# Kernel tuning notes

Measured on AMD Instinct MI355X. Metric: run time of the kernel, lower is better.

Reference implementation:

```python
import jax, jax.numpy as jnp
import numpy as np

BATCH, L, IN_DIM, HID, STATE, MLP, OUT, NUM_LAYERS = 16, 2048, 64, 256, 256, 1024, 128, 4
MAX_PHASE = 2.0 * np.pi


def setup_inputs() -> dict:
    key = jax.random.key(0)
    ks = iter(jax.random.split(key, 32))
    x = jax.random.normal(next(ks), (BATCH, L, IN_DIM), dtype=jnp.float32)
    # embedding Linear(IN_DIM -> HID)
    emb_W = jax.random.normal(next(ks), (HID, IN_DIM), dtype=jnp.float32) / np.sqrt(IN_DIM)
    emb_b = jnp.zeros((HID,), dtype=jnp.float32)
    # LRU params per layer (r_min=0, r_max=1, max_phase=2pi)
    u1 = jax.random.uniform(next(ks), (NUM_LAYERS, STATE), minval=1e-4, maxval=1.0)
    u2 = jax.random.uniform(next(ks), (NUM_LAYERS, STATE), minval=1e-4, maxval=1.0)
    nu_log = jnp.log(-0.5 * jnp.log(u1))
    theta_log = jnp.log(MAX_PHASE * u2)
    lam_abs = jnp.exp(-jnp.exp(nu_log))
    gamma_log = jnp.log(jnp.sqrt(1.0 - lam_abs ** 2))
    B_re = jax.random.normal(next(ks), (NUM_LAYERS, STATE, HID)) / np.sqrt(2 * HID)
    B_im = jax.random.normal(next(ks), (NUM_LAYERS, STATE, HID)) / np.sqrt(2 * HID)
    C_re = jax.random.normal(next(ks), (NUM_LAYERS, HID, STATE)) / np.sqrt(STATE)
    C_im = jax.random.normal(next(ks), (NUM_LAYERS, HID, STATE)) / np.sqrt(STATE)
    D = jax.random.normal(next(ks), (NUM_LAYERS, HID))
    # block MLP: Linear(STATE->MLP), GELU, Linear(MLP->HID)
    Wh = jax.random.normal(next(ks), (NUM_LAYERS, MLP, STATE)) / np.sqrt(STATE)
    bh = jnp.zeros((NUM_LAYERS, MLP), dtype=jnp.float32)
    Wo = jax.random.normal(next(ks), (NUM_LAYERS, HID, MLP)) / np.sqrt(MLP)
    bo = jnp.zeros((NUM_LAYERS, HID), dtype=jnp.float32)
    # output Linear(HID -> OUT)
    out_W = jax.random.normal(next(ks), (OUT, HID), dtype=jnp.float32) / np.sqrt(HID)
    out_b = jnp.zeros((OUT,), dtype=jnp.float32)
    return {"x": x, "emb_W": emb_W, "emb_b": emb_b, "nu_log": nu_log,
            "theta_log": theta_log, "gamma_log": gamma_log, "B_re": B_re,
            "B_im": B_im, "C_re": C_re, "C_im": C_im, "D": D,
            "Wh": Wh, "bh": bh, "Wo": Wo, "bo": bo,
            "out_W": out_W, "out_b": out_b}


def _binop(ei, ej):
    a_i, bu_i = ei
    a_j, bu_j = ej
    return a_j * a_i, a_j * bu_i + bu_j


def _lru(x, nu, th, gl, Bre, Bim, Cre, Cim, D):
    # x: (B, L, H) real; state diag recurrence in complex64
    lam = jnp.exp(-jnp.exp(nu) + 1j * jnp.exp(th))               # (S,)
    B_norm = (Bre + 1j * Bim) * jnp.exp(gl)[:, None]             # (S, H)
    Bu = jnp.einsum("blh,sh->bls", x.astype(B_norm.dtype), B_norm)  # (B, L, S)
    Lam = jnp.broadcast_to(lam, Bu.shape)
    _, states = jax.lax.associative_scan(_binop, (Lam, Bu), axis=1)
    C = Cre + 1j * Cim                                           # (H, S)
    y = jnp.einsum("bls,hs->blh", states, C).real + D * x        # (B, L, H)
    return y


def reference(x, emb_W, emb_b, nu_log, theta_log, gamma_log, B_re, B_im,
              C_re, C_im, D, Wh, bh, Wo, bo, out_W, out_b):
    h = x @ emb_W.T + emb_b                                      # (B, L, HID)
    for l in range(NUM_LAYERS):
        y = _lru(h, nu_log[l], theta_log[l], gamma_log[l],
                 B_re[l], B_im[l], C_re[l], C_im[l], D[l])
        z = jax.nn.gelu(y @ Wh[l].T + bh[l], approximate=False)  # exact GELU as torch
        h = z @ Wo[l].T + bo[l] + y                              # residual
    return h @ out_W.T + out_b                                   # (B, L, OUT)
```

## Files before the change

### kernel.cpp

```cpp
#include <hip/hip_runtime.h>
#include <hip/hip_bf16.h>
#include <math.h>

typedef __hip_bfloat16 bf16;
typedef __attribute__((ext_vector_type(8))) short bf16x8;
typedef __attribute__((ext_vector_type(4))) float f32x4;

#define BATCH   16
#define SEQLEN  2048
#define INDIM   64
#define HIDD    256
#define STATE_D 256
#define MLPD    1024
#define OUTD    128
#define NLAYERS 4
#define M_TOK   (BATCH*SEQLEN)
#define CHUNK   64
#define NCHUNK  (SEQLEN/CHUNK)

__device__ float g_carry[512*512];
__device__ bf16  g_hb [(size_t)M_TOK*256];
__device__ bf16  g_yb [(size_t)M_TOK*256];
__device__ bf16  g_bub[(size_t)M_TOK*512];
__device__ bf16  g_Bnb[NLAYERS*512*256];
__device__ bf16  g_Cwb[NLAYERS*256*512];
__device__ bf16  g_Whb[NLAYERS*1024*256];
__device__ bf16  g_Wob[NLAYERS*256*1024];

#define SB_HB  0
#define SB_YB  1
#define SB_BUB 2
#define SB_BNB 4
#define SB_CWB 5
#define SB_WHB 6
#define SB_WOB 7

__device__ __forceinline__ bf16* bufb(int sel){
  switch(sel){
    case SB_HB:  return g_hb;  case SB_YB:  return g_yb;
    case SB_BUB: return g_bub;
    case SB_BNB: return g_Bnb; case SB_CWB: return g_Cwb;
    case SB_WHB: return g_Whb; default:     return g_Wob; }
}

__device__ __forceinline__ void gld_lds16(const void* g, void* l){
  __builtin_amdgcn_global_load_lds(
      (const __attribute__((address_space(1))) unsigned int*)g,
      (__attribute__((address_space(3))) unsigned int*)l, 16, 0, 0);
}

__device__ __forceinline__ float fast_gelu(float v){
  const float x  = v * 0.70710678118654752f;
  const float ax = fabsf(x);
  const float t  = __builtin_amdgcn_rcpf(fmaf(0.3275911f, ax, 1.0f));
  float p = fmaf(t, 1.061405429f, -1.453152027f);
  p = fmaf(t, p, 1.421413741f);
  p = fmaf(t, p, -0.284496736f);
  p = fmaf(t, p, 0.254829592f);
  p = p * t;
  const float e = __expf(-ax * ax);
  const float erf_ax = fmaf(-p, e, 1.0f);
  const float erf_x  = copysignf(erf_ax, x);
  return 0.5f * v * (1.0f + erf_x);
}

__device__ __forceinline__ unsigned int bf2_add(unsigned int a, unsigned int b){
  float alo = __uint_as_float(a << 16), ahi = __uint_as_float(a & 0xffff0000u);
  float blo = __uint_as_float(b << 16), bhi = __uint_as_float(b & 0xffff0000u);
  bf16 l = __float2bfloat16(alo + blo);
  bf16 h = __float2bfloat16(ahi + bhi);
  return (unsigned int)(*reinterpret_cast<unsigned short*>(&l))
       | ((unsigned int)(*reinterpret_cast<unsigned short*>(&h)) << 16);
}

__device__ __forceinline__ void lam_of(const float* __restrict__ nu_log,
                                       const float* __restrict__ th_log,
                                       int s, float& lr, float& li)
{
  float nu  = expf(nu_log[s]);
  float th  = expf(th_log[s]);
  float mag = expf(-nu);
  lr = mag * cosf(th);
  li = mag * sinf(th);
}

#define RPSTR 136

template<int ACT, int FLAGS>
__global__ __launch_bounds__(256, 4) void mfma_gemm(
    int aSel, int lda, int wSel, int wOff, int ldw,
    int oSel, int ldc,
    const float* __restrict__ bias,
    int rSel, int ldres,
    const float* __restrict__ dscale,
    int K,
    const float* __restrict__ nu_log,
    const float* __restrict__ th_log)
{
  const bf16* A = bufb(aSel);
  const bf16* W = bufb(wSel) + wOff;
  bf16* OB = bufb(oSel);
  const bf16* res = (rSel >= 0) ? bufb(rSel) : nullptr;

  __shared__ __align__(16) unsigned short lds[18432];
  unsigned short* As = lds;
  unsigned short* Ws = lds + 6144;

  const int gx = gridDim.x;
  const int nwg = gx * gridDim.y;
  const int orig = blockIdx.y * gx + blockIdx.x;
  const int q = nwg >> 3, r = nwg & 7;
  const int xcd = orig & 7, idx = orig >> 3;
  const int wg = (xcd < r ? xcd*(q+1) : r*(q+1) + (xcd-r)*q) + idx;
  const int bx = wg % gx, by = wg / gx;

  const int tid  = threadIdx.x;
  const int row0 = by * 64, col0 = bx * 128;
  const int lane = tid & 63;
  const int m16  = lane & 15, quad = lane >> 4;
  const int wv   = tid >> 6;
  const int wm   = (wv & 1) * 32, wn = (wv >> 1) * 64;

  const int rlo = wv*16 + (lane >> 2);
  const int sg  = ((lane & 3) ^ ((rlo >> 1) & 3)) * 8;
  const bf16* ga = &A[(size_t)(row0 + rlo)*lda + sg];
  const bf16* gw = &W[(size_t)(col0 + rlo)*ldw + sg];
  const size_t w64 = (size_t)64 * ldw;

  auto STAGE = [&](int bb, int k0){
    unsigned short* Ab = As + bb*2048;
    unsigned short* Wb = Ws + bb*4096;
    gld_lds16(ga + k0,       Ab + wv*512);
    gld_lds16(gw + k0,       Wb + wv*512);
    gld_lds16(gw + k0 + w64, Wb + 2048 + wv*512);
  };

  f32x4 acc[2][4] = {};
  const int nt = K >> 5;

  STAGE(0, 0); STAGE(1, 32);

  int b = 0;
  for (int t = 0; t < nt; ++t){
    if (t + 1 < nt) asm volatile("s_waitcnt vmcnt(3)" ::: "memory");
    else            asm volatile("s_waitcnt vmcnt(0)" ::: "memory");
    __builtin_amdgcn_s_barrier();

    if (t + 2 < nt){
      const int st = (b == 0) ? 2 : b - 1;
      STAGE(st, (t + 2) << 5);
    }

    const unsigned short* Ab = As + b*2048;
    const unsigned short* Wb = Ws + b*4096;
    bf16x8 af[2], wf[4];
    #pragma unroll
    for (int i = 0; i < 2; i++){
      const int rA = wm + 16*i + m16;
      af[i] = *reinterpret_cast<const bf16x8*>(&Ab[rA*32 + ((quad ^ ((rA>>1)&3))<<3)]);
    }
    #pragma unroll
    for (int j = 0; j < 4; j++){
      const int rW = wn + 16*j + m16;
      wf[j] = *reinterpret_cast<const bf16x8*>(&Wb[rW*32 + ((quad ^ ((rW>>1)&3))<<3)]);
    }
    asm volatile("s_waitcnt lgkmcnt(0)" ::: "memory");
    __builtin_amdgcn_sched_barrier(0);

    __builtin_amdgcn_s_setprio(1);
    #pragma unroll
    for (int i = 0; i < 2; i++)
      #pragma unroll
      for (int j = 0; j < 4; j++)
        acc[i][j] = __builtin_amdgcn_mfma_f32_16x16x32_bf16(af[i], wf[j], acc[i][j], 0, 0, 0);
    __builtin_amdgcn_s_setprio(0);

    b = (b == 2) ? 0 : b + 1;
  }
  __builtin_amdgcn_s_barrier();

  #pragma unroll
  for (int i = 0; i < 2; i++){
    #pragma unroll
    for (int j = 0; j < 4; j++){
      const int lcol = wn + 16*j + m16;
      const int col  = col0 + lcol;
      #pragma unroll
      for (int r2 = 0; r2 < 4; r2++){
        const int lrow = wm + 16*i + quad*4 + r2;
        const int row  = row0 + lrow;
        float v = acc[i][j][r2];
        if (FLAGS & 1) v += bias[col];
        if (ACT == 1)  v = fast_gelu(v);
        if (FLAGS & 2) v += __bfloat162float(res[(size_t)row*ldres + col]);
        if (FLAGS & 4) v += dscale[col] * __bfloat162float(res[(size_t)row*ldres + col]);
        bf16 bv = __float2bfloat16(v);
        lds[lrow*RPSTR + lcol] = *reinterpret_cast<unsigned short*>(&bv);
      }
    }
  }
  __syncthreads();

  {
    const int rr  = tid >> 4;
    const int c16 = (tid & 15) * 8;
    #pragma unroll
    for (int s = 0; s < 4; s++){
      const int orow = s*16 + rr;
      uint4 d = *reinterpret_cast<const uint4*>(&lds[orow*RPSTR + c16]);
      *reinterpret_cast<uint4*>(OB + (size_t)(row0 + orow)*ldc + col0 + c16) = d;
    }
  }

  if (FLAGS & 8){
    if (tid < 64){
      const int sglob = (col0 >> 1) + tid;
      float lr, li; lam_of(nu_log, th_log, sglob, lr, li);
      float ar = 0.f, ai = 0.f;
      for (int t = 0; t < CHUNK; t++){
        unsigned int pr = *reinterpret_cast<const unsigned int*>(&lds[t*RPSTR + 2*tid]);
        float br = __uint_as_float(pr << 16);
        float bi = __uint_as_float(pr & 0xffff0000u);
        float nr = fmaf(lr, ar, fmaf(-li, ai, br));
        float ni = fmaf(lr, ai, fmaf( li, ar, bi));
        ar = nr; ai = ni;
      }
      g_carry[(size_t)by*512 + 2*sglob]     = ar;
      g_carry[(size_t)by*512 + 2*sglob + 1] = ai;
    }
  }
}

__global__ __launch_bounds__(512, 4) void fused_mlp(
    int whOff, int woOff,
    const float* __restrict__ bh, const float* __restrict__ bo)
{
  const bf16* Wh = g_Whb + whOff;
  const bf16* Wo = g_Wob + woOff;

  __shared__ __align__(16) unsigned short As[3*2048];
  __shared__ __align__(16) unsigned short Ws[3*8192];
  __shared__ __align__(16) unsigned short zbuf[64*132];

  const int tid  = threadIdx.x;
  const int row0 = blockIdx.x * 64;
  const int lane = tid & 63;
  const int m16  = lane & 15, quad = lane >> 4;
  const int wv   = tid >> 6;
  const int wm   = (wv & 3) * 16;
  const int wnA  = (wv >> 2) * 64;
  const int wnB  = (wv >> 2) * 128;

  const int lsub = lane >> 2;
  const int rloA = (wv & 3) * 16 + lsub;
  const int sgA  = ((lane & 3) ^ ((rloA >> 1) & 3)) * 8;
  const int rloW = wv * 16 + lsub;
  const int sgW  = ((lane & 3) ^ ((rloW >> 1) & 3)) * 8;

  const bf16* ga = g_yb + (size_t)(row0 + rloA)*HIDD + sgA;

  f32x4 accB[8] = {};

  for (int mc = 0; mc < 8; ++mc){
    const bf16* gwh = Wh + (size_t)(mc*128 + rloW)*HIDD + sgW;

    auto STAGE_A = [&](int b, int k0){
      gld_lds16(ga + k0,  As + b*2048 + (wv & 3)*512);
      gld_lds16(gwh + k0, Ws + b*8192 + wv*512);
    };
    auto STAGE_B = [&](int b, int ks){
      #pragma unroll
      for (int g = 0; g < 2; g++)
        gld_lds16(Wo + (size_t)(g*128 + rloW)*MLPD + mc*128 + ks*32 + sgW,
                  Ws + b*8192 + g*4096 + wv*512);
    };

    f32x4 accA[4] = {};
    STAGE_A(0, 0); STAGE_A(1, 32);
    int b = 0;
    for (int t = 0; t < 8; ++t){
      if (t + 1 < 8) asm volatile("s_waitcnt vmcnt(2)" ::: "memory");
      else           asm volatile("s_waitcnt vmcnt(0)" ::: "memory");
      __builtin_amdgcn_s_barrier();
      if (t + 2 < 8){
        const int st = (b == 0) ? 2 : b - 1;
        STAGE_A(st, (t + 2) << 5);
      }
      const unsigned short* Ab = As + b*2048;
      const unsigned short* Wb = Ws + b*8192;
      bf16x8 af, wf[4];
      { const int rA = wm + m16;
        af = *reinterpret_cast<const bf16x8*>(&Ab[rA*32 + ((quad ^ ((rA>>1)&3))<<3)]); }
      #pragma unroll
      for (int j = 0; j < 4; j++){
        const int rW = wnA + 16*j + m16;
        wf[j] = *reinterpret_cast<const bf16x8*>(&Wb[rW*32 + ((quad ^ ((rW>>1)&3))<<3)]);
      }
      asm volatile("s_waitcnt lgkmcnt(0)" ::: "memory");
      __builtin_amdgcn_sched_barrier(0);
      __builtin_amdgcn_s_setprio(1);
      #pragma unroll
      for (int j = 0; j < 4; j++)
        accA[j] = __builtin_amdgcn_mfma_f32_16x16x32_bf16(af, wf[j], accA[j], 0, 0, 0);
      __builtin_amdgcn_s_setprio(0);
      b = (b == 2) ? 0 : b + 1;
    }
    STAGE_B(2, 0); STAGE_B(0, 1);

    #pragma unroll
    for (int j = 0; j < 4; j++){
      const int lcol = wnA + 16*j + m16;
      const float bb = bh[mc*128 + lcol];
      #pragma unroll
      for (int r2 = 0; r2 < 4; r2++){
        const int lrow = wm + quad*4 + r2;
        float v = fast_gelu(accA[j][r2] + bb);
        bf16 bv = __float2bfloat16(v);
        zbuf[lrow*132 + lcol] = *reinterpret_cast<unsigned short*>(&bv);
      }
    }
    asm volatile("s_waitcnt lgkmcnt(0)" ::: "memory");
    __builtin_amdgcn_sched_barrier(0);
    __builtin_amdgcn_s_barrier();
    __builtin_amdgcn_sched_barrier(0);

    for (int ks = 0; ks < 4; ++ks){
      const int rb = (ks + 2) % 3;
      if (ks + 1 < 4) asm volatile("s_waitcnt vmcnt(2)" ::: "memory");
      else            asm volatile("s_waitcnt vmcnt(0)" ::: "memory");
      __builtin_amdgcn_s_barrier();
      if (ks + 2 < 4) STAGE_B((ks + 1) % 3, ks + 2);
      const unsigned short* Wb = Ws + rb*8192;
      bf16x8 af, wf[8];
      { const int rA = wm + m16;
        af = *reinterpret_cast<const bf16x8*>(&zbuf[rA*132 + ks*32 + quad*8]); }
      #pragma unroll
      for (int j = 0; j < 8; j++){
        const int rW = wnB + 16*j + m16;
        wf[j] = *reinterpret_cast<const bf16x8*>(&Wb[rW*32 + ((quad ^ ((rW>>1)&3))<<3)]);
      }
      asm volatile("s_waitcnt lgkmcnt(0)" ::: "memory");
      __builtin_amdgcn_sched_barrier(0);
      __builtin_amdgcn_s_setprio(1);
      #pragma unroll
      for (int j = 0; j < 8; j++)
        accB[j] = __builtin_amdgcn_mfma_f32_16x16x32_bf16(af, wf[j], accB[j], 0, 0, 0);
      __builtin_amdgcn_s_setprio(0);
    }
  }

  #pragma unroll
  for (int n = 0; n < 2; n++){
    asm volatile("s_waitcnt lgkmcnt(0)" ::: "memory");
    __builtin_amdgcn_sched_barrier(0);
    __builtin_amdgcn_s_barrier();
    __builtin_amdgcn_sched_barrier(0);
    if ((wv >> 2) == n){
      #pragma unroll
      for (int j = 0; j < 8; j++){
        const int lcol = 16*j + m16;
        const float bb = bo[n*128 + lcol];
        #pragma unroll
        for (int r2 = 0; r2 < 4; r2++){
          const int lrow = wm + quad*4 + r2;
          float v = accB[j][r2] + bb;
          bf16 bv = __float2bfloat16(v);
          zbuf[lrow*132 + lcol] = *reinterpret_cast<unsigned short*>(&bv);
        }
      }
    }
    asm volatile("s_waitcnt lgkmcnt(0)" ::: "memory");
    __builtin_amdgcn_sched_barrier(0);
    __builtin_amdgcn_s_barrier();
    __builtin_amdgcn_sched_barrier(0);
    const int rr = tid >> 4, c16 = (tid & 15) * 8;
    #pragma unroll
    for (int s = 0; s < 2; s++){
      const int orow = s*32 + rr;
      uint4 hv = *reinterpret_cast<const uint4*>(&zbuf[orow*132 + c16]);
      const size_t go = (size_t)(row0 + orow)*HIDD + n*128 + c16;
      uint4 yv = *reinterpret_cast<const uint4*>(g_yb + go);
      uint4 o;
      o.x = bf2_add(hv.x, yv.x); o.y = bf2_add(hv.y, yv.y);
      o.z = bf2_add(hv.z, yv.z); o.w = bf2_add(hv.w, yv.w);
      *reinterpret_cast<uint4*>(g_hb + go) = o;
    }
  }
}

__global__ __launch_bounds__(256) void emb_gemm(
    const float* __restrict__ x, const float* __restrict__ W,
    const float* __restrict__ b)
{
  __shared__ __align__(16) float Asx[16][68];
  __shared__ __align__(16) float Wsx[16][68];
  const int tid = threadIdx.x;
  const int tx = tid & 15, ty = tid >> 4;
  const int row0 = blockIdx.y * 64, col0 = blockIdx.x * 64;
  const int lc = tid & 15, lr = tid >> 4;
  float acc[4][4] = {};
  for (int k0 = 0; k0 < INDIM; k0 += 16){
    #pragma unroll
    for (int i = 0; i < 4; i++){
      Asx[lc][lr + 16*i] = x[(size_t)(row0 + lr + 16*i)*INDIM + k0 + lc];
      Wsx[lc][lr + 16*i] = W[(size_t)(col0 + lr + 16*i)*INDIM + k0 + lc];
    }
    __syncthreads();
    #pragma unroll
    for (int k = 0; k < 16; k++){
      float4 av = *reinterpret_cast<const float4*>(&Asx[k][ty*4]);
      float4 bv = *reinterpret_cast<const float4*>(&Wsx[k][tx*4]);
      float a[4] = {av.x, av.y, av.z, av.w};
      float b2[4] = {bv.x, bv.y, bv.z, bv.w};
      #pragma unroll
      for (int i = 0; i < 4; i++)
        #pragma unroll
        for (int j = 0; j < 4; j++)
          acc[i][j] = fmaf(a[i], b2[j], acc[i][j]);
    }
    __syncthreads();
  }
  #pragma unroll
  for (int i = 0; i < 4; i++){
    const int r = row0 + ty*4 + i;
    #pragma unroll
    for (int j = 0; j < 4; j++){
      const int cn = col0 + tx*4 + j;
      g_hb[(size_t)r*HIDD + cn] = __float2bfloat16(acc[i][j] + b[cn]);
    }
  }
}

__global__ __launch_bounds__(256) void out_gemm(
    const float* __restrict__ W, const float* __restrict__ b,
    float* __restrict__ out)
{
  __shared__ __align__(16) float Asx[16][68];
  __shared__ __align__(16) float Wsx[16][68];
  const int tid = threadIdx.x;
  const int tx = tid & 15, ty = tid >> 4;
  const int row0 = blockIdx.y * 64, col0 = blockIdx.x * 64;
  const int lc = tid & 15, lr = tid >> 4;
  float acc[4][4] = {};
  for (int k0 = 0; k0 < HIDD; k0 += 16){
    #pragma unroll
    for (int i = 0; i < 4; i++){
      Asx[lc][lr + 16*i] = __bfloat162float(g_hb[(size_t)(row0 + lr + 16*i)*HIDD + k0 + lc]);
      Wsx[lc][lr + 16*i] = W[(size_t)(col0 + lr + 16*i)*HIDD + k0 + lc];
    }
    __syncthreads();
    #pragma unroll
    for (int k = 0; k < 16; k++){
      float4 av = *reinterpret_cast<const float4*>(&Asx[k][ty*4]);
      float4 bv = *reinterpret_cast<const float4*>(&Wsx[k][tx*4]);
      float a[4] = {av.x, av.y, av.z, av.w};
      float b2[4] = {bv.x, bv.y, bv.z, bv.w};
      #pragma unroll
      for (int i = 0; i < 4; i++)
        #pragma unroll
        for (int j = 0; j < 4; j++)
          acc[i][j] = fmaf(a[i], b2[j], acc[i][j]);
    }
    __syncthreads();
  }
  #pragma unroll
  for (int i = 0; i < 4; i++){
    const int r = row0 + ty*4 + i;
    #pragma unroll
    for (int j = 0; j < 4; j++){
      const int cn = col0 + tx*4 + j;
      out[(size_t)r*OUTD + cn] = acc[i][j] + b[cn];
    }
  }
}

__global__ __launch_bounds__(256) void scan_fix(
    const float* __restrict__ nu_log, const float* __restrict__ th_log)
{
  const int blk = blockIdx.x;
  const int c   = blk & (NCHUNK - 1);
  const int s   = threadIdx.x;
  float lr, li; lam_of(nu_log, th_log, s, lr, li);
  float cr = 0.f, ci = 0.f;
  if (c > 0){
    float Tr = lr, Ti = li;
    #pragma unroll
    for (int i = 0; i < 6; i++){ float nr = Tr*Tr - Ti*Ti; Ti = 2.f*Tr*Ti; Tr = nr; }
    const int bstart = blk - c;
    for (int j = 0; j < c; j++){
      float2 e = *reinterpret_cast<const float2*>(&g_carry[(size_t)(bstart + j)*512 + 2*s]);
      float nr = fmaf(Tr, cr, fmaf(-Ti, ci, e.x));
      float ni = fmaf(Tr, ci, fmaf( Ti, cr, e.y));
      cr = nr; ci = ni;
    }
  }
  float ar = cr, ai = ci;
  unsigned int* pb = reinterpret_cast<unsigned int*>(g_bub) + (size_t)blk*CHUNK*256 + s;
  for (int t = 0; t < CHUNK; t++){
    unsigned int pr = pb[(size_t)t*256];
    float br = __uint_as_float(pr << 16);
    float bi = __uint_as_float(pr & 0xffff0000u);
    float nr = fmaf(lr, ar, fmaf(-li, ai, br));
    float ni = fmaf(lr, ai, fmaf( li, ar, bi));
    ar = nr; ai = ni;
    bf16 hr = __float2bfloat16(ar), hi2 = __float2bfloat16(ai);
    unsigned int w = (unsigned int)(*reinterpret_cast<unsigned short*>(&hr))
                   | ((unsigned int)(*reinterpret_cast<unsigned short*>(&hi2)) << 16);
    pb[(size_t)t*256] = w;
  }
}

__global__ __launch_bounds__(256) void pack_B(
    const float* __restrict__ Bre, const float* __restrict__ Bim,
    const float* __restrict__ gl)
{
  int idx = blockIdx.x * 256 + threadIdx.x;
  int l = idx >> 16, within = idx & 65535;
  int s = within >> 8, h = within & 255;
  float g = expf(gl[l*STATE_D + s]);
  g_Bnb[(size_t)l*131072 + (size_t)(2*s  )*256 + h] = __float2bfloat16(Bre[idx] * g);
  g_Bnb[(size_t)l*131072 + (size_t)(2*s+1)*256 + h] = __float2bfloat16(Bim[idx] * g);
}

__global__ __launch_bounds__(256) void pack_C(
    const float* __restrict__ Cre, const float* __restrict__ Cim)
{
  int idx = blockIdx.x * 256 + threadIdx.x;
  int l = idx >> 16, within = idx & 65535;
  int h = within >> 8, s = within & 255;
  g_Cwb[(size_t)l*131072 + (size_t)h*512 + 2*s]     = __float2bfloat16( Cre[idx]);
  g_Cwb[(size_t)l*131072 + (size_t)h*512 + 2*s + 1] = __float2bfloat16(-Cim[idx]);
}

__global__ __launch_bounds__(256) void conv_bf16(
    const float* __restrict__ src, int dstSel, int n)
{
  int i = blockIdx.x * 256 + threadIdx.x;
  if (i < n) bufb(dstSel)[i] = __float2bfloat16(src[i]);
}

extern "C" void kernel_launch(void* const* d_in, const int* in_sizes, int n_in,
                              void* d_out, int out_size, void* d_ws, size_t ws_size,
                              hipStream_t stream)
{
  (void)d_ws; (void)ws_size; (void)out_size; (void)n_in; (void)in_sizes;
  const float* x      = (const float*)d_in[0];
  const float* emb_W  = (const float*)d_in[1];
  const float* emb_b  = (const float*)d_in[2];
  const float* nu_log = (const float*)d_in[3];
  const float* th_log = (const float*)d_in[4];
  const float* ga_log = (const float*)d_in[5];
  const float* B_re   = (const float*)d_in[6];
  const float* B_im   = (const float*)d_in[7];
  const float* C_re   = (const float*)d_in[8];
  const float* C_im   = (const float*)d_in[9];
  const float* Dv     = (const float*)d_in[10];
  const float* Wh     = (const float*)d_in[11];
  const float* bh     = (const float*)d_in[12];
  const float* Wo     = (const float*)d_in[13];
  const float* bo     = (const float*)d_in[14];
  const float* out_W  = (const float*)d_in[15];
  const float* out_b  = (const float*)d_in[16];

  const dim3 blk(256);

  pack_B<<<dim3(NLAYERS*256), blk, 0, stream>>>(B_re, B_im, ga_log);
  pack_C<<<dim3(NLAYERS*256), blk, 0, stream>>>(C_re, C_im);
  conv_bf16<<<dim3(NLAYERS*1024), blk, 0, stream>>>(Wh, SB_WHB, NLAYERS*262144);
  conv_bf16<<<dim3(NLAYERS*1024), blk, 0, stream>>>(Wo, SB_WOB, NLAYERS*262144);

  emb_gemm<<<dim3(HIDD/64, M_TOK/64), blk, 0, stream>>>(x, emb_W, emb_b);

  for (int l = 0; l < NLAYERS; l++){
    mfma_gemm<0, 8><<<dim3(4, M_TOK/64), blk, 0, stream>>>(
        SB_HB, HIDD, SB_BNB, l*131072, HIDD, SB_BUB, 512,
        nullptr, -1, 0, nullptr, HIDD,
        nu_log + l*STATE_D, th_log + l*STATE_D);

    scan_fix<<<dim3(M_TOK/CHUNK), blk, 0, stream>>>(nu_log + l*STATE_D, th_log + l*STATE_D);

    mfma_gemm<0, 4><<<dim3(2, M_TOK/64), blk, 0, stream>>>(
        SB_BUB, 512, SB_CWB, l*131072, 512, SB_YB, HIDD,
        nullptr, SB_HB, HIDD, Dv + l*HIDD, 512, nullptr, nullptr);

    fused_mlp<<<dim3(M_TOK/64), dim3(512), 0, stream>>>(
        l*262144, l*262144, bh + l*MLPD, bo + l*HIDD);
  }

  out_gemm<<<dim3(OUTD/64, M_TOK/64), blk, 0, stream>>>(out_W, out_b, (float*)d_out);
}
```

Baseline: 711.0 us.

## Keep the y tile resident in LDS and double-buffer MLP weight tiles

The fused MLP kernel now loads the 64x256 y tile into LDS once per block instead of re-streaming it for each of the 8 MLP chunks. Weight staging moves from a triple-buffered 32-wide K pipeline to a double-buffered pipeline with 64-wide K tiles, and the next chunk's Wh tile is prefetched during the Wo phase. The z buffer swaps padding for an XOR swizzle. This removes repeated global reads of y and halves the barriers in the first GEMM, at the cost of full vmcnt(0) waits, which shorten how far loads run ahead. LDS per block changes, which may affect occupancy.

```diff
diff --git a/kernel.cpp b/kernel.cpp
--- a/kernel.cpp
+++ b/kernel.cpp
@@ -238,9 +238,9 @@
   const bf16* Wh = g_Whb + whOff;
   const bf16* Wo = g_Wob + woOff;
 
-  __shared__ __align__(16) unsigned short As[3*2048];
-  __shared__ __align__(16) unsigned short Ws[3*8192];
-  __shared__ __align__(16) unsigned short zbuf[64*132];
+  __shared__ __align__(16) unsigned short ybuf[64*256];
+  __shared__ __align__(16) unsigned short Ws[2*8192];
+  __shared__ __align__(16) unsigned short zbuf[64*128];
 
   const int tid  = threadIdx.x;
   const int row0 = blockIdx.x * 64;
@@ -251,89 +251,110 @@
   const int wnA  = (wv >> 2) * 64;
   const int wnB  = (wv >> 2) * 128;
 
-  const int lsub = lane >> 2;
-  const int rloA = (wv & 3) * 16 + lsub;
-  const int sgA  = ((lane & 3) ^ ((rloA >> 1) & 3)) * 8;
-  const int rloW = wv * 16 + lsub;
-  const int sgW  = ((lane & 3) ^ ((rloW >> 1) & 3)) * 8;
-
-  const bf16* ga = g_yb + (size_t)(row0 + rloA)*HIDD + sgA;
+  auto STAGE_Y = [&](){
+    #pragma unroll
+    for (int s = 0; s < 4; s++){
+      const int blkrow = (wv*4 + s)*2;
+      const int row = blkrow + (lane >> 5);
+      const int g   = lane & 31;
+      const int gs  = (g & ~7) | ((g & 7) ^ (row & 7));
+      gld_lds16(g_yb + (size_t)(row0 + row)*HIDD + gs*8,
+                ybuf + (wv*4 + s)*512);
+    }
+  };
+  auto STAGE_WH = [&](int b, int mc, int kt){
+    #pragma unroll
+    for (int s = 0; s < 2; s++){
+      const int trow = wv*16 + s*8 + (lane >> 3);
+      const int g    = lane & 7;
+      const int gs   = g ^ (trow & 7);
+      gld_lds16(Wh + (size_t)(mc*128 + trow)*HIDD + kt*64 + gs*8,
+                Ws + b*8192 + wv*1024 + s*512);
+    }
+  };
+  auto STAGE_WO = [&](int b, int mc, int ks){
+    #pragma unroll
+    for (int s = 0; s < 2; s++){
+      const int trow = wv*32 + s*16 + (lane >> 2);
+      const int g    = lane & 3;
+      const int gs   = g ^ ((trow >> 1) & 3);
+      gld_lds16(Wo + (size_t)trow*MLPD + mc*128 + ks*32 + gs*8,
+                Ws + b*8192 + wv*1024 + s*512);
+    }
+  };
 
   f32x4 accB[8] = {};
 
+  STAGE_Y();
+  STAGE_WH(0, 0, 0);
+
   for (int mc = 0; mc < 8; ++mc){
-    const bf16* gwh = Wh + (size_t)(mc*128 + rloW)*HIDD + sgW;
-
-    auto STAGE_A = [&](int b, int k0){
-      gld_lds16(ga + k0,  As + b*2048 + (wv & 3)*512);
-      gld_lds16(gwh + k0, Ws + b*8192 + wv*512);
-    };
-    auto STAGE_B = [&](int b, int ks){
-      #pragma unroll
-      for (int g = 0; g < 2; g++)
-        gld_lds16(Wo + (size_t)(g*128 + rloW)*MLPD + mc*128 + ks*32 + sgW,
-                  Ws + b*8192 + g*4096 + wv*512);
-    };
-
     f32x4 accA[4] = {};
-    STAGE_A(0, 0); STAGE_A(1, 32);
-    int b = 0;
-    for (int t = 0; t < 8; ++t){
-      if (t + 1 < 8) asm volatile("s_waitcnt vmcnt(2)" ::: "memory");
-      else           asm volatile("s_waitcnt vmcnt(0)" ::: "memory");
+    for (int kt = 0; kt < 4; ++kt){
+      asm volatile("s_waitcnt vmcnt(0)" ::: "memory");
       __builtin_amdgcn_s_barrier();
-      if (t + 2 < 8){
-        const int st = (b == 0) ? 2 : b - 1;
-        STAGE_A(st, (t + 2) << 5);
-      }
-      const unsigned short* Ab = As + b*2048;
-      const unsigned short* Wb = Ws + b*8192;
-      bf16x8 af, wf[4];
-      { const int rA = wm + m16;
-        af = *reinterpret_cast<const bf16x8*>(&Ab[rA*32 + ((quad ^ ((rA>>1)&3))<<3)]); }
+      if (kt < 3) STAGE_WH((kt + 1) & 1, mc, kt + 1);
+      else        STAGE_WO(0, mc, 0);
+
+      const unsigned short* Wb = Ws + (kt & 1)*8192;
+      const int rA = wm + m16;
+      bf16x8 af[2], wf[8];
+      #pragma unroll
+      for (int ik = 0; ik < 2; ik++)
+        af[ik] = *reinterpret_cast<const bf16x8*>(
+            &ybuf[rA*256 + (kt*8 + ((ik*4 + quad) ^ (rA & 7)))*8]);
       #pragma unroll
       for (int j = 0; j < 4; j++){
         const int rW = wnA + 16*j + m16;
-        wf[j] = *reinterpret_cast<const bf16x8*>(&Wb[rW*32 + ((quad ^ ((rW>>1)&3))<<3)]);
+        #pragma unroll
+        for (int ik = 0; ik < 2; ik++)
+          wf[j*2 + ik] = *reinterpret_cast<const bf16x8*>(
+              &Wb[rW*64 + (((ik*4 + quad) ^ (rW & 7)))*8]);
       }
       asm volatile("s_waitcnt lgkmcnt(0)" ::: "memory");
       __builtin_amdgcn_sched_barrier(0);
       __builtin_amdgcn_s_setprio(1);
       #pragma unroll
       for (int j = 0; j < 4; j++)
-        accA[j] = __builtin_amdgcn_mfma_f32_16x16x32_bf16(af, wf[j], accA[j], 0, 0, 0);
+        #pragma unroll
+        for (int ik = 0; ik < 2; ik++)
+          accA[j] = __builtin_amdgcn_mfma_f32_16x16x32_bf16(af[ik], wf[j*2 + ik], accA[j], 0, 0, 0);
       __builtin_amdgcn_s_setprio(0);
-      b = (b == 2) ? 0 : b + 1;
-    }
-    STAGE_B(2, 0); STAGE_B(0, 1);
+    }
 
     #pragma unroll
     for (int j = 0; j < 4; j++){
       const int lcol = wnA + 16*j + m16;
       const float bb = bh[mc*128 + lcol];
+      const int G = lcol >> 3, c7 = lcol & 7;
       #pragma unroll
       for (int r2 = 0; r2 < 4; r2++){
-        const int lrow = wm + quad*4 + r2;
+        const int row = wm + quad*4 + r2;
+        const int Gs  = (G & 8) | ((G & 7) ^ (row & 7));
         float v = fast_gelu(accA[j][r2] + bb);
         bf16 bv = __float2bfloat16(v);
-        zbuf[lrow*132 + lcol] = *reinterpret_cast<unsigned short*>(&bv);
+        zbuf[row*128 + Gs*8 + c7] = *reinterpret_cast<unsigned short*>(&bv);
       }
     }
-    asm volatile("s_waitcnt lgkmcnt(0)" ::: "memory");
+    asm volatile("s_waitcnt vmcnt(0) lgkmcnt(0)" ::: "memory");
     __builtin_amdgcn_sched_barrier(0);
     __builtin_amdgcn_s_barrier();
     __builtin_amdgcn_sched_barrier(0);
 
     for (int ks = 0; ks < 4; ++ks){
-      const int rb = (ks + 2) % 3;
-      if (ks + 1 < 4) asm volatile("s_waitcnt vmcnt(2)" ::: "memory");
-      else            asm volatile("s_waitcnt vmcnt(0)" ::: "memory");
-      __builtin_amdgcn_s_barrier();
-      if (ks + 2 < 4) STAGE_B((ks + 1) % 3, ks + 2);
-      const unsigned short* Wb = Ws + rb*8192;
+      if (ks > 0){
+        asm volatile("s_waitcnt vmcnt(0)" ::: "memory");
+        __builtin_amdgcn_s_barrier();
+      }
+      if (ks < 3)      STAGE_WO((ks + 1) & 1, mc, ks + 1);
+      else if (mc < 7) STAGE_WH(0, mc + 1, 0);
+
+      const unsigned short* Wb = Ws + (ks & 1)*8192;
+      const int rA = wm + m16;
+      const int G  = ks*4 + quad;
       bf16x8 af, wf[8];
-      { const int rA = wm + m16;
-        af = *reinterpret_cast<const bf16x8*>(&zbuf[rA*132 + ks*32 + quad*8]); }
+      af = *reinterpret_cast<const bf16x8*>(
+          &zbuf[rA*128 + ((G & 8) | ((G & 7) ^ (rA & 7)))*8]);
       #pragma unroll
       for (int j = 0; j < 8; j++){
         const int rW = wnB + 16*j + m16;
@@ -360,12 +381,14 @@
       for (int j = 0; j < 8; j++){
         const int lcol = 16*j + m16;
         const float bb = bo[n*128 + lcol];
+        const int G = lcol >> 3, c7 = lcol & 7;
         #pragma unroll
         for (int r2 = 0; r2 < 4; r2++){
-          const int lrow = wm + quad*4 + r2;
+          const int row = wm + quad*4 + r2;
+          const int Gs  = (G & 8) | ((G & 7) ^ (row & 7));
           float v = accB[j][r2] + bb;
           bf16 bv = __float2bfloat16(v);
-          zbuf[lrow*132 + lcol] = *reinterpret_cast<unsigned short*>(&bv);
+          zbuf[row*128 + Gs*8 + c7] = *reinterpret_cast<unsigned short*>(&bv);
         }
       }
     }
@@ -373,12 +396,13 @@
     __builtin_amdgcn_sched_barrier(0);
     __builtin_amdgcn_s_barrier();
     __builtin_amdgcn_sched_barrier(0);
-    const int rr = tid >> 4, c16 = (tid & 15) * 8;
+    const int rr = tid >> 4, g = tid & 15;
     #pragma unroll
     for (int s = 0; s < 2; s++){
       const int orow = s*32 + rr;
-      uint4 hv = *reinterpret_cast<const uint4*>(&zbuf[orow*132 + c16]);
-      const size_t go = (size_t)(row0 + orow)*HIDD + n*128 + c16;
+      const int Gs = (g & 8) | ((g & 7) ^ (orow & 7));
+      uint4 hv = *reinterpret_cast<const uint4*>(&zbuf[orow*128 + Gs*8]);
+      const size_t go = (size_t)(row0 + orow)*HIDD + n*128 + g*8;
       uint4 yv = *reinterpret_cast<const uint4*>(g_yb + go);
       uint4 o;
       o.x = bf2_add(hv.x, yv.x); o.y = bf2_add(hv.y, yv.y);
```

Measured after the change: 777.0 us. +9.3%, slower.
